# Kernel optimization log

Hardware: AMD Instinct MI355X
Metric: run time of the kernel (lower is better)

Reference implementation:

```python
import jax, jax.numpy as jnp
import numpy as np
import math

B, S, DM, H = 4, 2048, 1024, 16
HD = DM // H

def setup_inputs() -> dict:
    key = jax.random.key(0)
    ks = jax.random.split(key, 12)
    def lin(k, din, dout):
        bound = 1.0 / math.sqrt(din)
        kw, kb = jax.random.split(k)
        W = jax.random.uniform(kw, (din, dout), jnp.float32, -bound, bound)
        b = jax.random.uniform(kb, (dout,), jnp.float32, -bound, bound)
        return W, b
    Wq, bq = lin(ks[0], DM, DM)
    Wk, bk = lin(ks[1], DM, DM)
    Wv, bv = lin(ks[2], DM, DM)
    Wo, bo = lin(ks[3], DM, DM)
    return {
        "Q": jax.random.normal(ks[4], (B, S, DM), jnp.float32),
        "K": jax.random.normal(ks[5], (B, S, DM), jnp.float32),
        "V": jax.random.normal(ks[6], (B, S, DM), jnp.float32),
        "mask": jnp.ones((B, S), jnp.int32),
        "Wq": Wq, "bq": bq, "Wk": Wk, "bk": bk,
        "Wv": Wv, "bv": bv, "Wo": Wo, "bo": bo,
    }

def reference(Q, K, V, mask, Wq, bq, Wk, bk, Wv, bv, Wo, bo):
    N, qlen, dm = Q.shape
    klen = K.shape[1]
    q = (Q @ Wq + bq).reshape(N, qlen, H, HD)
    k = (K @ Wk + bk).reshape(N, klen, H, HD)
    v = (V @ Wv + bv).reshape(N, klen, H, HD)
    # scores: [B, q, H, k]
    dot = jnp.einsum('bqhd,bkhd->bqhk', q, k) / math.sqrt(HD)
    # mask is 2-D (N, klen): broadcast as (N, 1, 1, klen); positions where mask==0 are masked
    m = (mask == 0)[:, None, None, :]
    dot = jnp.where(m, -jnp.inf, dot)
    weights = jax.nn.softmax(dot.astype(jnp.float32), axis=-1).astype(dot.dtype)
    out = jnp.einsum('bqhk,bkhd->bqhd', weights, v).reshape(N, qlen, dm)
    return out @ Wo + bo
```

## Files before the change

### kernel.cpp

```cpp
#include <hip/hip_runtime.h>
#include <math.h>

#define B_  4
#define S_  2048
#define DM_ 1024
#define H_  16
#define HD_ 64

typedef float f32x4 __attribute__((ext_vector_type(4)));
typedef short bf16x8 __attribute__((ext_vector_type(8)));

#define MFMA16(a, b, c) __builtin_amdgcn_mfma_f32_16x16x32_bf16((a), (b), (c), 0, 0, 0)

static __device__ __forceinline__ unsigned short f2bf(float f) {
    union { float f; unsigned int i; } c; c.f = f;
    unsigned int u = c.i;
    return (unsigned short)((u + 0x7fffu + ((u >> 16) & 1u)) >> 16);
}
static __device__ __forceinline__ unsigned int f2u(float f) {
    union { float f; unsigned int u; } c; c.f = f; return c.u;
}

static __device__ __forceinline__ void async16(const void* g, void* l) {
    __builtin_amdgcn_global_load_lds(
        (__attribute__((address_space(1))) void*)(void*)g,
        (__attribute__((address_space(3))) void*)l, 16, 0, 0);
}

__global__ __launch_bounds__(256) void cast3_bf16(
    const float* __restrict__ q, const float* __restrict__ k,
    const float* __restrict__ v,
    unsigned short* __restrict__ qo, unsigned short* __restrict__ ko,
    unsigned short* __restrict__ vo) {
    const int z = blockIdx.z;
    const float* in = z == 0 ? q : (z == 1 ? k : v);
    unsigned short* out = z == 0 ? qo : (z == 1 ? ko : vo);
    int idx = (blockIdx.x * 256 + threadIdx.x) * 8;
    float4 a = *(const float4*)(in + idx);
    float4 b = *(const float4*)(in + idx + 4);
    *(ushort4*)(out + idx)     = make_ushort4(f2bf(a.x), f2bf(a.y), f2bf(a.z), f2bf(a.w));
    *(ushort4*)(out + idx + 4) = make_ushort4(f2bf(b.x), f2bf(b.y), f2bf(b.z), f2bf(b.w));
}

__global__ __launch_bounds__(256) void maskprep(
    const int* __restrict__ mask, float* __restrict__ maddf,
    unsigned int* __restrict__ flags) {
    int i = blockIdx.x * 256 + threadIdx.x;
    int m = mask[i];
    maddf[i] = m ? 0.f : -__builtin_inff();
    unsigned long long bal = __ballot(m != 0);
    if ((threadIdx.x & 63) == 0)
        flags[i >> 6] = (bal == 0xFFFFFFFFFFFFFFFFull) ? 1u : 0u;
}

__global__ __launch_bounds__(256) void wcast4_t(
    const float* __restrict__ w0, const float* __restrict__ w1,
    const float* __restrict__ w2, const float* __restrict__ w3,
    unsigned short* __restrict__ o0, unsigned short* __restrict__ o1,
    unsigned short* __restrict__ o2, unsigned short* __restrict__ o3) {
    __shared__ float tile[64][65];
    const int z = blockIdx.z;
    const float* W = z == 0 ? w0 : (z == 1 ? w1 : (z == 2 ? w2 : w3));
    unsigned short* Wt = z == 0 ? o0 : (z == 1 ? o1 : (z == 2 ? o2 : o3));
    const int t = threadIdx.x;
    const int k0 = blockIdx.y * 64, n0 = blockIdx.x * 64;
    const int r = t >> 4, c4 = (t & 15) * 4;
    #pragma unroll
    for (int s = 0; s < 4; ++s) {
        float4 f = *(const float4*)(W + (size_t)(k0 + s * 16 + r) * DM_ + n0 + c4);
        tile[s * 16 + r][c4 + 0] = f.x; tile[s * 16 + r][c4 + 1] = f.y;
        tile[s * 16 + r][c4 + 2] = f.z; tile[s * 16 + r][c4 + 3] = f.w;
    }
    __syncthreads();
    #pragma unroll
    for (int s = 0; s < 4; ++s) {
        int n = s * 16 + r;
        ushort4 o = make_ushort4(f2bf(tile[c4 + 0][n]), f2bf(tile[c4 + 1][n]),
                                 f2bf(tile[c4 + 2][n]), f2bf(tile[c4 + 3][n]));
        *(ushort4*)(Wt + (size_t)(n0 + n) * DM_ + k0 + c4) = o;
    }
}

static __device__ __forceinline__ void gemm_body(
    const unsigned short* __restrict__ A,
    const unsigned short* __restrict__ Wt,
    const float* __restrict__ bias,
    void* __restrict__ outp, int mode, float oscale,
    unsigned short* As, unsigned short* Bs)
{
    const int t = threadIdx.x;
    const int w = t >> 6, l = t & 63;
    const int quad = l >> 4, l16 = l & 15;
    const int wr = w >> 1, wc = w & 1;
    const int m0 = blockIdx.y * 128, n0 = blockIdx.x * 128;

    const int srow8 = l >> 3;
    const int sch   = (l & 7) ^ srow8;
    const unsigned short* ag = A  + (size_t)(m0 + w * 32 + srow8) * DM_ + sch * 8;
    const unsigned short* bg = Wt + (size_t)(n0 + w * 32 + srow8) * DM_ + sch * 8;

    const f32x4 fz = {0.f, 0.f, 0.f, 0.f};
    f32x4 acc[4][4];
    #pragma unroll
    for (int i = 0; i < 4; ++i)
        #pragma unroll
        for (int j = 0; j < 4; ++j) acc[i][j] = fz;

    const int rsw = l16 & 7;
    for (int k0 = 0; k0 < DM_; k0 += 64) {
        __syncthreads();
        #pragma unroll
        for (int s = 0; s < 4; ++s) {
            async16(ag + k0 + (size_t)(s * 8) * DM_, &As[(w * 32 + s * 8) * 64]);
            async16(bg + k0 + (size_t)(s * 8) * DM_, &Bs[(w * 32 + s * 8) * 64]);
        }
        __syncthreads();
        #pragma unroll
        for (int c = 0; c < 2; ++c) {
            const int csw = ((c * 4 + quad) ^ rsw) * 8;
            bf16x8 af[4], bfr[4];
            #pragma unroll
            for (int i = 0; i < 4; ++i)
                af[i] = *(const bf16x8*)&As[(wr * 64 + i * 16 + l16) * 64 + csw];
            #pragma unroll
            for (int j = 0; j < 4; ++j)
                bfr[j] = *(const bf16x8*)&Bs[(wc * 64 + j * 16 + l16) * 64 + csw];
            #pragma unroll
            for (int i = 0; i < 4; ++i)
                #pragma unroll
                for (int j = 0; j < 4; ++j)
                    acc[i][j] = MFMA16(af[i], bfr[j], acc[i][j]);
        }
    }

    float bv[4];
    #pragma unroll
    for (int j = 0; j < 4; ++j) bv[j] = bias[n0 + wc * 64 + j * 16 + l16];

    if (mode == 2) {
        float* out = (float*)outp;
        #pragma unroll
        for (int i = 0; i < 4; ++i)
            #pragma unroll
            for (int j = 0; j < 4; ++j) {
                int col = n0 + wc * 64 + j * 16 + l16;
                #pragma unroll
                for (int r = 0; r < 4; ++r) {
                    int row = m0 + wr * 64 + i * 16 + quad * 4 + r;
                    out[(size_t)row * DM_ + col] = acc[i][j][r] + bv[j];
                }
            }
    } else if (mode == 0) {
        unsigned short* out = (unsigned short*)outp;
        #pragma unroll
        for (int i = 0; i < 4; ++i)
            #pragma unroll
            for (int j = 0; j < 4; ++j) {
                int col = n0 + wc * 64 + j * 16 + l16;
                int h = col >> 6, d = col & 63;
                #pragma unroll
                for (int r = 0; r < 4; ++r) {
                    int row = m0 + wr * 64 + i * 16 + quad * 4 + r;
                    int bb = row >> 11, ss = row & (S_ - 1);
                    out[(((size_t)bb * H_ + h) * S_ + ss) * HD_ + d] =
                        f2bf((acc[i][j][r] + bv[j]) * oscale);
                }
            }
    } else {
        unsigned short* out = (unsigned short*)outp;
        #pragma unroll
        for (int i = 0; i < 4; ++i)
            #pragma unroll
            for (int j = 0; j < 4; ++j) {
                int col = n0 + wc * 64 + j * 16 + l16;
                int h = col >> 6, d = col & 63;
                int row0 = m0 + wr * 64 + i * 16 + quad * 4;
                int bb = row0 >> 11, ss = row0 & (S_ - 1);
                ushort4 o = make_ushort4(f2bf(acc[i][j][0] + bv[j]),
                                         f2bf(acc[i][j][1] + bv[j]),
                                         f2bf(acc[i][j][2] + bv[j]),
                                         f2bf(acc[i][j][3] + bv[j]));
                *(ushort4*)(out + (((size_t)bb * H_ + h) * HD_ + d) * S_ + ss) = o;
            }
    }
}

__global__ __launch_bounds__(256) void gemm_qkv3(
    const unsigned short* __restrict__ Qc, const unsigned short* __restrict__ Kc,
    const unsigned short* __restrict__ Vc,
    const unsigned short* __restrict__ Wqt, const unsigned short* __restrict__ Wkt,
    const unsigned short* __restrict__ Wvt,
    const float* __restrict__ bq, const float* __restrict__ bk,
    const float* __restrict__ bvp,
    unsigned short* __restrict__ qh, unsigned short* __restrict__ kh,
    unsigned short* __restrict__ vth)
{
    __shared__ unsigned short As[128 * 64];
    __shared__ unsigned short Bs[128 * 64];
    const int z = blockIdx.z;
    const unsigned short* A  = z == 0 ? Qc  : (z == 1 ? Kc  : Vc);
    const unsigned short* Wt = z == 0 ? Wqt : (z == 1 ? Wkt : Wvt);
    const float* bias        = z == 0 ? bq  : (z == 1 ? bk  : bvp);
    void* out                = z == 0 ? (void*)qh : (z == 1 ? (void*)kh : (void*)vth);
    const float qsc = 0.18033688011112042f;
    gemm_body(A, Wt, bias, out, z == 2 ? 1 : 0, z == 0 ? qsc : 1.0f, As, Bs);
}

__global__ __launch_bounds__(256) void gemm_omfma(
    const unsigned short* __restrict__ A, const unsigned short* __restrict__ Wt,
    const float* __restrict__ bias, float* __restrict__ out)
{
    __shared__ unsigned short As[128 * 64];
    __shared__ unsigned short Bs[128 * 64];
    gemm_body(A, Wt, bias, out, 2, 1.0f, As, Bs);
}

template<bool MASKED>
static __device__ __forceinline__ void softmax_store(
    const f32x4* sc, const float (*madd)[4], unsigned short* Pg,
    int l16, int quad, int rsw, float& lout)
{
    float lacc = 0.f;
    #pragma unroll
    for (int kk = 0; kk < 4; ++kk) {
        int kb = (kk * 2 + (quad >> 1)) ^ rsw;
        #pragma unroll
        for (int rp = 0; rp < 2; ++rp) {
            float a0 = sc[kk][rp * 2 + 0], a1 = sc[kk][rp * 2 + 1];
            if (MASKED) { a0 += madd[kk][rp * 2 + 0]; a1 += madd[kk][rp * 2 + 1]; }
            float p0 = __builtin_amdgcn_exp2f(a0);
            float p1 = __builtin_amdgcn_exp2f(a1);
            unsigned int pk = __builtin_amdgcn_perm(f2u(p1), f2u(p0), 0x07060302u);
            lacc += p0 + p1;
            *(unsigned int*)&Pg[l16 * 64 + kb * 8 + (quad & 1) * 4 + rp * 2] = pk;
        }
    }
    lout += lacc;
}

__global__ __launch_bounds__(256) void attn_mfma(
    const unsigned short* __restrict__ q,
    const unsigned short* __restrict__ k,
    const unsigned short* __restrict__ vt,
    const float* __restrict__ maddf,
    const unsigned int* __restrict__ flags,
    unsigned short* __restrict__ out)
{
    __shared__ unsigned short Ks[2][64 * 64];
    __shared__ unsigned short Vs[2][64 * 64];
    __shared__ unsigned short Ps[4][16 * 64];
    const int t = threadIdx.x;
    const int w = t >> 6, l = t & 63;
    const int quad = l >> 4, l16 = l & 15;

    const int bid = blockIdx.x;
    const int swz = (bid & 7) * 128 + (bid >> 3);
    const int qb = swz & 15, h = (swz >> 4) & 15, b = swz >> 8;
    const int q0 = qb * 128;
    const size_t hb = ((size_t)b * H_ + h) * S_;

    const int srow8 = l >> 3;
    const int sch   = (l & 7) ^ srow8;
    const int rsw   = l16 & 7;

    const unsigned short* qg = q + (hb + q0) * HD_;
    bf16x8 qf[2][2];
    #pragma unroll
    for (int g = 0; g < 2; ++g)
        #pragma unroll
        for (int c = 0; c < 2; ++c)
            qf[g][c] = *(const bf16x8*)(qg +
                (size_t)(w * 32 + g * 16 + l16) * HD_ + (c * 4 + quad) * 8);

    const f32x4 fz = {0.f, 0.f, 0.f, 0.f};
    f32x4 o[2][4];
    float lr[2] = {0.f, 0.f};
    #pragma unroll
    for (int g = 0; g < 2; ++g)
        #pragma unroll
        for (int jv = 0; jv < 4; ++jv) o[g][jv] = fz;

    const unsigned short* kg0 = k + hb * HD_;
    const unsigned short* vg0 = vt + ((size_t)b * H_ + h) * HD_ * S_;
    unsigned short* Pg = &Ps[w][0];

    auto stage = [&](int d, int kt) {
        #pragma unroll
        for (int s = 0; s < 2; ++s) {
            int r0 = w * 16 + s * 8;
            int rr = r0 + srow8;
            async16(kg0 + (size_t)(kt * 64 + rr) * HD_ + sch * 8, &Ks[d][r0 * 64]);
            async16(vg0 + (size_t)rr * S_ + kt * 64 + sch * 8, &Vs[d][r0 * 64]);
        }
    };

    stage(0, 0);
    int cur = 0;
    for (int kt = 0; kt < S_ / 64; ++kt) {
        __syncthreads();
        if (kt + 1 < S_ / 64) stage(cur ^ 1, kt + 1);

        const int allv = flags[b * (S_ / 64) + kt];
        float madd[4][4];
        if (!allv) {
            #pragma unroll
            for (int kk = 0; kk < 4; ++kk) {
                float4 mv = *(const float4*)&maddf[(size_t)b * S_ + kt * 64 + kk * 16 + quad * 4];
                madd[kk][0] = mv.x; madd[kk][1] = mv.y;
                madd[kk][2] = mv.z; madd[kk][3] = mv.w;
            }
        }

        const unsigned short* Kc = &Ks[cur][0];
        const unsigned short* Vc = &Vs[cur][0];
        bf16x8 kf[4][2], vfr[4][2];
        #pragma unroll
        for (int kk = 0; kk < 4; ++kk) {
            int row = kk * 16 + l16;
            #pragma unroll
            for (int c = 0; c < 2; ++c)
                kf[kk][c] = *(const bf16x8*)&Kc[row * 64 + (((c * 4 + quad) ^ rsw) * 8)];
        }
        #pragma unroll
        for (int jv = 0; jv < 4; ++jv) {
            int row = jv * 16 + l16;
            #pragma unroll
            for (int c = 0; c < 2; ++c)
                vfr[jv][c] = *(const bf16x8*)&Vc[row * 64 + (((c * 4 + quad) ^ rsw) * 8)];
        }

        #pragma unroll
        for (int g = 0; g < 2; ++g) {
            f32x4 sc[4];
            #pragma unroll
            for (int kk = 0; kk < 4; ++kk) sc[kk] = fz;
            #pragma unroll
            for (int kk = 0; kk < 4; ++kk) {
                sc[kk] = MFMA16(kf[kk][0], qf[g][0], sc[kk]);
                sc[kk] = MFMA16(kf[kk][1], qf[g][1], sc[kk]);
            }
            if (allv) softmax_store<false>(sc, madd, Pg, l16, quad, rsw, lr[g]);
            else      softmax_store<true >(sc, madd, Pg, l16, quad, rsw, lr[g]);

            bf16x8 pa0 = *(const bf16x8*)&Pg[l16 * 64 + ((quad ^ rsw) * 8)];
            bf16x8 pa1 = *(const bf16x8*)&Pg[l16 * 64 + (((4 + quad) ^ rsw) * 8)];
            #pragma unroll
            for (int jv = 0; jv < 4; ++jv) {
                o[g][jv] = MFMA16(pa0, vfr[jv][0], o[g][jv]);
                o[g][jv] = MFMA16(pa1, vfr[jv][1], o[g][jv]);
            }
        }
        cur ^= 1;
    }

    #pragma unroll
    for (int g = 0; g < 2; ++g) {
        float ls = lr[g];
        ls += __shfl_xor(ls, 16);
        ls += __shfl_xor(ls, 32);
        float inv = 1.0f / ls;
        float invr[4];
        #pragma unroll
        for (int r = 0; r < 4; ++r)
            invr[r] = __shfl(inv, (l & 48) | (quad * 4 + r));
        #pragma unroll
        for (int jv = 0; jv < 4; ++jv) {
            int col = h * HD_ + jv * 16 + l16;
            #pragma unroll
            for (int r = 0; r < 4; ++r) {
                int row = q0 + w * 32 + g * 16 + quad * 4 + r;
                out[((size_t)b * S_ + row) * DM_ + col] = f2bf(o[g][jv][r] * invr[r]);
            }
        }
    }
}

extern "C" void kernel_launch(void* const* d_in, const int* in_sizes, int n_in,
                              void* d_out, int out_size, void* d_ws, size_t ws_size,
                              hipStream_t stream) {
    const float* Q    = (const float*)d_in[0];
    const float* K    = (const float*)d_in[1];
    const float* V    = (const float*)d_in[2];
    const int*   mask = (const int*)d_in[3];
    const float* Wq   = (const float*)d_in[4];
    const float* bq   = (const float*)d_in[5];
    const float* Wk   = (const float*)d_in[6];
    const float* bk   = (const float*)d_in[7];
    const float* Wv   = (const float*)d_in[8];
    const float* bv   = (const float*)d_in[9];
    const float* Wo   = (const float*)d_in[10];
    const float* bo   = (const float*)d_in[11];

    char* ws = (char*)d_ws;
    const size_t MB = 1024 * 1024;
    unsigned short* Qc  = (unsigned short*)(ws);
    unsigned short* Kc  = (unsigned short*)(ws + 16 * MB);
    unsigned short* Vc  = (unsigned short*)(ws + 32 * MB);
    unsigned short* Wqt = (unsigned short*)(ws + 48 * MB);
    unsigned short* Wkt = (unsigned short*)(ws + 50 * MB);
    unsigned short* Wvt = (unsigned short*)(ws + 52 * MB);
    unsigned short* Wot = (unsigned short*)(ws + 54 * MB);
    unsigned short* qh  = (unsigned short*)(ws + 56 * MB);
    unsigned short* kh  = (unsigned short*)(ws + 72 * MB);
    unsigned short* vth = (unsigned short*)(ws + 88 * MB);
    unsigned short* ao  = (unsigned short*)(ws + 104 * MB);
    float*          maddf = (float*)(ws + 120 * MB);
    unsigned int*   flagsb = (unsigned int*)(ws + 120 * MB + 64 * 1024);

    cast3_bf16<<<dim3(4096, 1, 3), 256, 0, stream>>>(Q, K, V, Qc, Kc, Vc);
    maskprep<<<dim3((B_ * S_) / 256), 256, 0, stream>>>(mask, maddf, flagsb);
    wcast4_t<<<dim3(16, 16, 4), 256, 0, stream>>>(Wq, Wk, Wv, Wo, Wqt, Wkt, Wvt, Wot);
    gemm_qkv3<<<dim3(DM_ / 128, (B_ * S_) / 128, 3), 256, 0, stream>>>(
        Qc, Kc, Vc, Wqt, Wkt, Wvt, bq, bk, bv, qh, kh, vth);
    attn_mfma<<<dim3((S_ / 128) * H_ * B_), 256, 0, stream>>>(
        qh, kh, vth, maddf, flagsb, ao);
    gemm_omfma<<<dim3(DM_ / 128, (B_ * S_) / 128), 256, 0, stream>>>(ao, Wot, bo, (float*)d_out);
}
```

Measured before the change: 363.5 us.

## Compute softmax row sums via MFMA with ones and split QK/PV phases

Drops the per-element VALU accumulation of softmax probabilities and instead gets the row sum by running the bf16 P tiles through extra MFMAs against a vector of ones. This also removes the cross-lane shuffles in the epilogue. The P staging buffer is doubled so both query groups' scores are computed and stored before the V fragments are loaded and the PV MFMAs run. setprio hints are added around the MFMA blocks. The cost is two extra MFMAs per group per tile and more LDS. Summing the bf16-rounded P rather than fp32 P changes the normalisation slightly.

```diff
diff --git a/kernel.cpp b/kernel.cpp
--- a/kernel.cpp
+++ b/kernel.cpp
@@ -218,9 +218,8 @@
 template<bool MASKED>
 static __device__ __forceinline__ void softmax_store(
     const f32x4* sc, const float (*madd)[4], unsigned short* Pg,
-    int l16, int quad, int rsw, float& lout)
+    int l16, int quad, int rsw)
 {
-    float lacc = 0.f;
     #pragma unroll
     for (int kk = 0; kk < 4; ++kk) {
         int kb = (kk * 2 + (quad >> 1)) ^ rsw;
@@ -231,11 +230,9 @@
             float p0 = __builtin_amdgcn_exp2f(a0);
             float p1 = __builtin_amdgcn_exp2f(a1);
             unsigned int pk = __builtin_amdgcn_perm(f2u(p1), f2u(p0), 0x07060302u);
-            lacc += p0 + p1;
             *(unsigned int*)&Pg[l16 * 64 + kb * 8 + (quad & 1) * 4 + rp * 2] = pk;
         }
     }
-    lout += lacc;
 }
 
 __global__ __launch_bounds__(256) void attn_mfma(
@@ -248,7 +245,7 @@
 {
     __shared__ unsigned short Ks[2][64 * 64];
     __shared__ unsigned short Vs[2][64 * 64];
-    __shared__ unsigned short Ps[4][16 * 64];
+    __shared__ unsigned short Ps[4][2][16 * 64];
     const int t = threadIdx.x;
     const int w = t >> 6, l = t & 63;
     const int quad = l >> 4, l16 = l & 15;
@@ -272,9 +269,12 @@
             qf[g][c] = *(const bf16x8*)(qg +
                 (size_t)(w * 32 + g * 16 + l16) * HD_ + (c * 4 + quad) * 8);
 
+    const bf16x8 onesf = {(short)0x3F80, (short)0x3F80, (short)0x3F80, (short)0x3F80,
+                          (short)0x3F80, (short)0x3F80, (short)0x3F80, (short)0x3F80};
+
     const f32x4 fz = {0.f, 0.f, 0.f, 0.f};
     f32x4 o[2][4];
-    float lr[2] = {0.f, 0.f};
+    f32x4 ol[2] = {fz, fz};
     #pragma unroll
     for (int g = 0; g < 2; ++g)
         #pragma unroll
@@ -282,7 +282,6 @@
 
     const unsigned short* kg0 = k + hb * HD_;
     const unsigned short* vg0 = vt + ((size_t)b * H_ + h) * HD_ * S_;
-    unsigned short* Pg = &Ps[w][0];
 
     auto stage = [&](int d, int kt) {
         #pragma unroll
@@ -312,8 +311,7 @@
         }
 
         const unsigned short* Kc = &Ks[cur][0];
-        const unsigned short* Vc = &Vs[cur][0];
-        bf16x8 kf[4][2], vfr[4][2];
+        bf16x8 kf[4][2];
         #pragma unroll
         for (int kk = 0; kk < 4; ++kk) {
             int row = kk * 16 + l16;
@@ -322,54 +320,59 @@
                 kf[kk][c] = *(const bf16x8*)&Kc[row * 64 + (((c * 4 + quad) ^ rsw) * 8)];
         }
         #pragma unroll
-        for (int jv = 0; jv < 4; ++jv) {
-            int row = jv * 16 + l16;
-            #pragma unroll
-            for (int c = 0; c < 2; ++c)
-                vfr[jv][c] = *(const bf16x8*)&Vc[row * 64 + (((c * 4 + quad) ^ rsw) * 8)];
-        }
-
-        #pragma unroll
         for (int g = 0; g < 2; ++g) {
             f32x4 sc[4];
             #pragma unroll
             for (int kk = 0; kk < 4; ++kk) sc[kk] = fz;
+            __builtin_amdgcn_s_setprio(1);
             #pragma unroll
             for (int kk = 0; kk < 4; ++kk) {
                 sc[kk] = MFMA16(kf[kk][0], qf[g][0], sc[kk]);
                 sc[kk] = MFMA16(kf[kk][1], qf[g][1], sc[kk]);
             }
-            if (allv) softmax_store<false>(sc, madd, Pg, l16, quad, rsw, lr[g]);
-            else      softmax_store<true >(sc, madd, Pg, l16, quad, rsw, lr[g]);
-
-            bf16x8 pa0 = *(const bf16x8*)&Pg[l16 * 64 + ((quad ^ rsw) * 8)];
-            bf16x8 pa1 = *(const bf16x8*)&Pg[l16 * 64 + (((4 + quad) ^ rsw) * 8)];
+            __builtin_amdgcn_s_setprio(0);
+            if (allv) softmax_store<false>(sc, madd, &Ps[w][g][0], l16, quad, rsw);
+            else      softmax_store<true >(sc, madd, &Ps[w][g][0], l16, quad, rsw);
+        }
+
+        const unsigned short* Vc = &Vs[cur][0];
+        bf16x8 vfr[4][2];
+        #pragma unroll
+        for (int jv = 0; jv < 4; ++jv) {
+            int row = jv * 16 + l16;
+            #pragma unroll
+            for (int c = 0; c < 2; ++c)
+                vfr[jv][c] = *(const bf16x8*)&Vc[row * 64 + (((c * 4 + quad) ^ rsw) * 8)];
+        }
+        #pragma unroll
+        for (int g = 0; g < 2; ++g) {
+            bf16x8 pa0 = *(const bf16x8*)&Ps[w][g][l16 * 64 + ((quad ^ rsw) * 8)];
+            bf16x8 pa1 = *(const bf16x8*)&Ps[w][g][l16 * 64 + (((4 + quad) ^ rsw) * 8)];
+            __builtin_amdgcn_s_setprio(1);
             #pragma unroll
             for (int jv = 0; jv < 4; ++jv) {
                 o[g][jv] = MFMA16(pa0, vfr[jv][0], o[g][jv]);
                 o[g][jv] = MFMA16(pa1, vfr[jv][1], o[g][jv]);
             }
+            ol[g] = MFMA16(pa0, onesf, ol[g]);
+            ol[g] = MFMA16(pa1, onesf, ol[g]);
+            __builtin_amdgcn_s_setprio(0);
         }
         cur ^= 1;
     }
 
     #pragma unroll
     for (int g = 0; g < 2; ++g) {
-        float ls = lr[g];
-        ls += __shfl_xor(ls, 16);
-        ls += __shfl_xor(ls, 32);
-        float inv = 1.0f / ls;
-        float invr[4];
-        #pragma unroll
-        for (int r = 0; r < 4; ++r)
-            invr[r] = __shfl(inv, (l & 48) | (quad * 4 + r));
+        float inv[4];
+        #pragma unroll
+        for (int r = 0; r < 4; ++r) inv[r] = 1.0f / ol[g][r];
         #pragma unroll
         for (int jv = 0; jv < 4; ++jv) {
             int col = h * HD_ + jv * 16 + l16;
             #pragma unroll
             for (int r = 0; r < 4; ++r) {
                 int row = q0 + w * 32 + g * 16 + quad * 4 + r;
-                out[((size_t)b * S_ + row) * DM_ + col] = f2bf(o[g][jv][r] * invr[r]);
+                out[((size_t)b * S_ + row) * DM_ + col] = f2bf(o[g][jv][r] * inv[r]);
             }
         }
     }
```

Result: no change. 357.3 us (-1.7%).
